# Performance work log

Measured on AMD Instinct MI355X. Metric: run time of the kernel, lower is better.

## Reference

```python
import jax, jax.numpy as jnp
import numpy as np

G, P, PO, TAU = 4, 32, 128, 2.0  # n_groups, spatial_points, out_points=P*out_multiplier, level-softmax temperature
STRIDES = (4.0, 8.0, 16.0, 32.0)
EPS = 1e-5

def _ln2(x):
    # LayerNorm over last two dims, no affine (F.layer_norm(x, x.shape[-2:]))
    mu = jnp.mean(x, axis=(-2, -1), keepdims=True)
    var = jnp.var(x, axis=(-2, -1), keepdims=True)
    return (x - mu) * jax.lax.rsqrt(var + EPS)

def _ln1(x, g, b):
    mu = jnp.mean(x, axis=-1, keepdims=True)
    var = jnp.var(x, axis=-1, keepdims=True)
    return (x - mu) * jax.lax.rsqrt(var + EPS) * g + b

def _bilinear(feat, xp, yp):
    # feat: (B,G,H,W,Ce); xp,yp: (B,N,G,P) pixel coords; grid_sample bilinear,
    # zero padding, align_corners=False semantics.
    B, Gg, H, W, Ce = feat.shape
    x0 = jnp.floor(xp); y0 = jnp.floor(yp)
    wx1 = xp - x0; wy1 = yp - y0
    b_idx = jnp.arange(B)[:, None, None, None]
    g_idx = jnp.arange(Gg)[None, None, :, None]
    def gather(xi, yi):
        valid = (xi >= 0) & (xi < W) & (yi >= 0) & (yi < H)
        xc = jnp.clip(xi, 0, W - 1).astype(jnp.int32)
        yc = jnp.clip(yi, 0, H - 1).astype(jnp.int32)
        return feat[b_idx, g_idx, yc, xc] * valid[..., None]
    v00 = gather(x0, y0); v10 = gather(x0 + 1.0, y0)
    v01 = gather(x0, y0 + 1.0); v11 = gather(x0 + 1.0, y0 + 1.0)
    wx0 = 1.0 - wx1; wy0 = 1.0 - wy1
    return (v00 * (wx0 * wy0)[..., None] + v10 * (wx1 * wy0)[..., None]
            + v01 * (wx0 * wy1)[..., None] + v11 * (wx1 * wy1)[..., None])

def _forward(queries, xyzr, feats, W_off, b_off, W_param, b_param, W_out, b_out, gamma, beta):
    B, N, D = queries.shape
    Ce = feats[0].shape[1] // G  # 64 channels per group
    # learned offsets -> sample points (make_sample_points)
    offset = (queries @ W_off + b_off).reshape(B, N, G, P, 3)
    xy = xyzr[..., :2]
    z = xyzr[..., 2]
    r = xyzr[..., 3:4]
    roi_wh = (2.0 ** xyzr[..., 2:3]) * (2.0 ** jnp.concatenate([-0.5 * r, 0.5 * r], axis=-1))  # (B,N,2)
    sample_xy = xy[:, :, None, None, :] + offset[..., :2] * roi_wh[:, :, None, None, :]  # (B,N,G,P,2)
    sample_z = z[:, :, None, None] + offset[..., 2]  # (B,N,G,P) log2 scale
    # soft level assignment across the FPN pyramid
    lvl_log = jnp.log2(jnp.asarray(STRIDES, dtype=queries.dtype))
    lw = jax.nn.softmax(-((sample_z[..., None] - lvl_log) ** 2) / TAU, axis=-1)  # (B,N,G,P,L)
    # SAMPLE4D (image mode, T=1): multi-scale group-wise bilinear gather, level-weighted sum
    sampled = jnp.zeros((B, N, G, P, Ce), queries.dtype)
    for l, feat in enumerate(feats):
        H, W = feat.shape[-2:]
        featg = feat.reshape(B, G, Ce, H, W).transpose(0, 1, 3, 4, 2)  # (B,G,H,W,Ce)
        xp = sample_xy[..., 0] / STRIDES[l] - 0.5
        yp = sample_xy[..., 1] / STRIDES[l] - 0.5
        sampled = sampled + _bilinear(featg, xp, yp) * lw[..., l, None]
    # AdaptiveMixing: per-query generated channel-mix M and point-mix S
    params = (queries @ W_param + b_param).reshape(B, N, G, -1)
    M = params[..., :Ce * Ce].reshape(B, N, G, Ce, Ce)
    S = params[..., Ce * Ce:].reshape(B, N, G, PO, P)
    h = jnp.einsum('bngpc,bngcd->bngpd', sampled, M)  # channel mixing
    h = jax.nn.relu(_ln2(h))
    h = jnp.einsum('bngqp,bngpd->bngqd', S, h)        # point mixing -> (B,N,G,PO,Ce)
    h = jax.nn.relu(_ln2(h))
    h = h.reshape(B, N, G * PO * Ce)
    q = queries + h @ W_out + b_out  # out_proj + residual
    return _ln1(q, gamma, beta)      # norm_s

def setup_inputs() -> dict:
    key = jax.random.key(0)
    ks = jax.random.split(key, 12)
    B, N, D, C = 2, 300, 256, 256
    HW = [(200, 336), (100, 168), (50, 84), (25, 42)]
    inp = {}
    inp['queries'] = jax.random.normal(ks[0], (B, N, D), jnp.float32)
    u = jax.random.uniform(ks[1], (B, N, 4), jnp.float32)
    inp['xyzr'] = jnp.stack([u[..., 0] * 1344.0, u[..., 1] * 800.0,
                             2.0 + 3.0 * u[..., 2], u[..., 3] - 0.5], axis=-1)
    for i, (H, W) in enumerate(HW):
        inp[f'feat{i}'] = jax.random.normal(ks[2 + i], (B, C, H, W), jnp.float32)
    npar = G * (64 * 64 + PO * P)  # 32768
    inp['W_off'] = jax.random.normal(ks[6], (D, G * P * 3), jnp.float32) * 0.02
    inp['b_off'] = jax.random.normal(ks[7], (G * P * 3,), jnp.float32) * 0.1
    inp['W_param'] = jax.random.normal(ks[8], (D, npar), jnp.float32) * (1.0 / np.sqrt(D))
    inp['b_param'] = jnp.zeros((npar,), jnp.float32)
    inp['W_out'] = jax.random.normal(ks[9], (G * PO * 64, D), jnp.float32) * (1.0 / np.sqrt(G * PO * 64))
    inp['b_out'] = jnp.zeros((D,), jnp.float32)
    inp['gamma'] = jnp.ones((D,), jnp.float32)
    inp['beta'] = jnp.zeros((D,), jnp.float32)
    return inp

def reference(queries, xyzr, feat0, feat1, feat2, feat3, W_off, b_off, W_param, b_param, W_out, b_out, gamma, beta):
    return _forward(queries, xyzr, (feat0, feat1, feat2, feat3),
                    W_off, b_off, W_param, b_param, W_out, b_out, gamma, beta)
```

## Files before the change

kernel.cpp:

```cpp
#include <hip/hip_runtime.h>
#include <hip/hip_bf16.h>

typedef short bf16x8 __attribute__((ext_vector_type(8)));
typedef float f32x4 __attribute__((ext_vector_type(4)));
typedef unsigned short u16x4 __attribute__((ext_vector_type(4)));

#define NQ 600
#define D 256
#define NPAR 32768
#define EPS 1e-5f
#define KSPLIT 32

#define OFF_OFFS     ((size_t)0)
#define OFF_QB       ((size_t)1048576)
#define OFF_WOFFT    ((size_t)1441792)
#define OFF_H        ((size_t)2097152)
#define OFF_WPT      ((size_t)2097152)
#define OFF_PARAMS   ((size_t)41418752)
#define OFF_KPART    ((size_t)41418752)
#define OFF_WOT      ((size_t)80740352)
#define OFF_FEATT    ((size_t)97517568)

#define PIX_PER_BG 89250

__device__ __forceinline__ void gload_lds16(const void* g, void* l) {
    __builtin_amdgcn_global_load_lds((const __attribute__((address_space(1))) unsigned int*)g,
                                     (__attribute__((address_space(3))) unsigned int*)l,
                                     16, 0, 0);
}
__device__ __forceinline__ float bf2f(unsigned short us) {
    union { unsigned u; float f; } cv; cv.u = ((unsigned)us) << 16; return cv.f;
}
__device__ __forceinline__ unsigned short f2bf(float f) {
    __hip_bfloat16 h = __float2bfloat16(f);
    return *(unsigned short*)&h;
}

__global__ __launch_bounds__(256) void k_mega_prep(
        const float* __restrict__ f0, const float* __restrict__ f1,
        const float* __restrict__ f2, const float* __restrict__ f3,
        const float* __restrict__ W_param, const float* __restrict__ W_out,
        const float* __restrict__ W_off, const float* __restrict__ q,
        __hip_bfloat16* __restrict__ featT,
        __hip_bfloat16* __restrict__ Wpt, __hip_bfloat16* __restrict__ Wot,
        __hip_bfloat16* __restrict__ Wofft, __hip_bfloat16* __restrict__ qb) {
    __shared__ __align__(16) float tile[64 * 66];
    int bidf = blockIdx.x;
    int t = threadIdx.x;
    if (bidf < 13000) {
        int bg = bidf / 1625, r = bidf % 1625;
        const float* in; int H, W, lvloff, y, x0;
        if (r < 1200)      { in = f0; H = 200; W = 336; lvloff = 0;     y = r / 6;  x0 = (r % 6) * 64; }
        else if (r < 1500) { r -= 1200; in = f1; H = 100; W = 168; lvloff = 67200; y = r / 3; x0 = (r % 3) * 64; }
        else if (r < 1600) { r -= 1500; in = f2; H = 50;  W = 84;  lvloff = 84000; y = r >> 1; x0 = (r & 1) * 64; }
        else               { r -= 1600; in = f3; H = 25;  W = 42;  lvloff = 88200; y = r;     x0 = 0; }
        int b = bg >> 2, g = bg & 3;
        const float* inb = in + ((size_t)(b * 256 + g * 64) * H + y) * W + x0;
        size_t HW = (size_t)H * W;
        #pragma unroll
        for (int rr = 0; rr < 8; rr++) {
            int qq = t + 256 * rr;
            int c = qq >> 5, xl = (qq & 31) * 2;
            if (x0 + xl < W) {
                float2 v = *(const float2*)(inb + (size_t)c * HW + xl);
                *(float2*)(tile + c * 66 + xl) = v;
            }
        }
        __syncthreads();
        __hip_bfloat16* ob = featT + ((size_t)bg * PIX_PER_BG + lvloff + (size_t)y * W + x0) * 64;
        #pragma unroll
        for (int r2 = 0; r2 < 2; r2++) {
            int task = t + 256 * r2;
            int xl = task >> 3, c8 = (task & 7) * 8;
            if (x0 + xl < W) {
                unsigned short o[8];
                #pragma unroll
                for (int i = 0; i < 8; i++) o[i] = f2bf(tile[(c8 + i) * 66 + xl]);
                *(bf16x8*)(ob + (size_t)xl * 64 + c8) = *(bf16x8*)o;
            }
        }
        return;
    }
    int idx = bidf - 13000;
    if (idx >= 16480) {
        int i = (idx - 16480) * 2048 + t * 8;
        float4 v0 = *(const float4*)(q + i);
        float4 v1 = *(const float4*)(q + i + 4);
        unsigned short o[8];
        o[0] = f2bf(v0.x); o[1] = f2bf(v0.y); o[2] = f2bf(v0.z); o[3] = f2bf(v0.w);
        o[4] = f2bf(v1.x); o[5] = f2bf(v1.y); o[6] = f2bf(v1.z); o[7] = f2bf(v1.w);
        *(bf16x8*)(qb + i) = *(bf16x8*)o;
        return;
    }
    const float* in; __hip_bfloat16* out; int R, C, bx, by;
    if (idx < 8192)       { in = W_param; out = Wpt;   R = 256;   C = 32768; bx = idx & 1023; by = idx >> 10; }
    else if (idx < 16384) { idx -= 8192;  in = W_out;  out = Wot; R = 32768; C = 256; bx = idx & 7; by = idx >> 3; }
    else                  { idx -= 16384; in = W_off;  out = Wofft; R = 256; C = 384; bx = idx % 12; by = idx / 12; }
    float (*tt)[33] = (float(*)[33])tile;
    int tx = t & 31, ty = t >> 5;
    int c = bx * 32 + tx;
    #pragma unroll
    for (int i = 0; i < 4; i++) {
        int rr = by * 32 + ty + i * 8;
        float v = 0.f;
        if (rr < R && c < C) v = in[(size_t)rr * C + c];
        tt[ty + i * 8][tx] = v;
    }
    __syncthreads();
    int r2 = by * 32 + tx;
    #pragma unroll
    for (int i = 0; i < 4; i++) {
        int c2 = bx * 32 + ty + i * 8;
        if (c2 < C && r2 < R) out[(size_t)c2 * R + r2] = __float2bfloat16(tt[tx][ty + i * 8]);
    }
}

__global__ __launch_bounds__(256) void k_gemm1_offs(const __hip_bfloat16* __restrict__ A,
                              const __hip_bfloat16* __restrict__ WofftB, const __hip_bfloat16* __restrict__ WptB,
                              const float* __restrict__ b_off, const float* __restrict__ b_param,
                              float* __restrict__ offs, __hip_bfloat16* __restrict__ params) {
    __shared__ __align__(16) char ldsB[65536];
    int id = blockIdx.x;
    bool isOff = id < 15;
    int m0, n0;
    const __hip_bfloat16* Bt;
    const float* bias;
    if (isOff) { m0 = (id % 5) * 128; n0 = (id / 5) * 128; Bt = WofftB; bias = b_off; }
    else { int i2 = id - 15; m0 = (i2 % 5) * 128; n0 = (i2 / 5) * 128; Bt = WptB; bias = b_param; }
    int t = threadIdx.x;
    int lane = t & 63, w = t >> 6;
    int la = lane & 15, lb = lane >> 4;

    const char* Bg = (const char*)Bt;
    #pragma unroll
    for (int r = 0; r < 16; r++) {
        int p = (r * 4 + w) * 64 + lane;
        int row = p >> 5, c16 = p & 31;
        int c16s = c16 ^ (row & 7);
        gload_lds16(Bg + (size_t)(n0 + row) * 512 + c16s * 16, ldsB + p * 16);
    }
    bf16x8 a[2][8];
    #pragma unroll
    for (int mi = 0; mi < 2; mi++) {
        int row = m0 + w * 32 + mi * 16 + la;
        row = row < NQ ? row : NQ - 1;
        #pragma unroll
        for (int ks = 0; ks < 8; ks++)
            a[mi][ks] = *(const bf16x8*)(A + (size_t)row * 256 + ks * 32 + lb * 8);
    }
    f32x4 acc[2][8];
    #pragma unroll
    for (int i = 0; i < 2; i++)
        #pragma unroll
        for (int j = 0; j < 8; j++) acc[i][j] = (f32x4)(0.f);
    __syncthreads();

    #pragma unroll
    for (int ks = 0; ks < 8; ks++) {
        bf16x8 b[8];
        #pragma unroll
        for (int ni = 0; ni < 8; ni++) {
            int row = ni * 16 + la;
            int c16s = (ks * 4 + lb) ^ (row & 7);
            b[ni] = *(const bf16x8*)(ldsB + row * 512 + c16s * 16);
        }
        #pragma unroll
        for (int mi = 0; mi < 2; mi++)
            #pragma unroll
            for (int ni = 0; ni < 8; ni++)
                acc[mi][ni] = __builtin_amdgcn_mfma_f32_16x16x32_bf16(a[mi][ks], b[ni], acc[mi][ni], 0, 0, 0);
    }
    #pragma unroll
    for (int mi = 0; mi < 2; mi++) {
        int rbase = m0 + w * 32 + mi * 16 + lb * 4;
        #pragma unroll
        for (int ni = 0; ni < 8; ni++) {
            int col = n0 + ni * 16 + la;
            float bv = bias[col];
            #pragma unroll
            for (int rg = 0; rg < 4; rg++) {
                int row = rbase + rg;
                if (row < NQ) {
                    if (isOff) offs[(size_t)row * 384 + col] = acc[mi][ni][rg] + bv;
                    else params[(size_t)row * NPAR + col] = __float2bfloat16(acc[mi][ni][rg] + bv);
                }
            }
        }
    }
}

#define MIX_SMP 0
#define MIX_MT  4096
#define MIX_SS  12288
#define MIX_H1T 20480
__device__ inline float2 blk_reduce2(float s, float ss, float* red, float norm) {
    __syncthreads();
    #pragma unroll
    for (int off = 32; off; off >>= 1) { s += __shfl_down(s, off); ss += __shfl_down(ss, off); }
    int wave = threadIdx.x >> 6, lane = threadIdx.x & 63;
    if (lane == 0) { red[wave * 2] = s; red[wave * 2 + 1] = ss; }
    __syncthreads();
    if (threadIdx.x == 0) {
        float a = 0.f, b = 0.f;
        #pragma unroll
        for (int i = 0; i < 4; i++) { a += red[2 * i]; b += red[2 * i + 1]; }
        red[8] = a * norm; red[9] = b * norm;
    }
    __syncthreads();
    return make_float2(red[8], red[9]);
}

__global__ __launch_bounds__(256) void k_sample_mix(const float* __restrict__ offs,
                      const float* __restrict__ xyzr,
                      const __hip_bfloat16* __restrict__ featT,
                      const __hip_bfloat16* __restrict__ params,
                      __hip_bfloat16* __restrict__ h) {
    __shared__ __align__(16) char lds[24576];
    __shared__ float smeta[32][8];
    __shared__ float red[16];
    int bid = blockIdx.x;
    int m = bid >> 2, g = bid & 3;
    int b = m / 300;
    int t = threadIdx.x;
    int lane = t & 63, w = t >> 6;
    int la = lane & 15, lb = lane >> 4;
    const __hip_bfloat16* pbase = params + (size_t)m * NPAR + g * 8192;

    #pragma unroll
    for (int r = 0; r < 2; r++) {
        int i = t + r * 256;
        int c = i >> 3, d0 = (i & 7) * 8;
        bf16x8 v = *(const bf16x8*)(pbase + i * 8);
        #pragma unroll
        for (int j = 0; j < 8; j++) {
            int d = d0 + j;
            int addr = MIX_MT + d * 128 + ((c >> 3) ^ (d & 7)) * 16 + (c & 7) * 2;
            *(unsigned short*)(lds + addr) = ((unsigned short*)&v)[j];
        }
    }
    #pragma unroll
    for (int r = 0; r < 2; r++) {
        int i = t + r * 256;
        int qr = i >> 2, c16 = i & 3;
        bf16x8 v = *(const bf16x8*)(pbase + 4096 + i * 8);
        *(bf16x8*)(lds + MIX_SS + qr * 64 + (c16 ^ (qr & 3)) * 16) = v;
    }
    if (t < 32) {
        int p = t;
        const float* op = offs + (size_t)m * 384 + (g * 32 + p) * 3;
        float o0 = op[0], o1 = op[1], o2 = op[2];
        float cx = xyzr[m * 4 + 0], cy = xyzr[m * 4 + 1], z = xyzr[m * 4 + 2], rr = xyzr[m * 4 + 3];
        smeta[p][0] = cx + o0 * exp2f(z - 0.5f * rr);
        smeta[p][1] = cy + o1 * exp2f(z + 0.5f * rr);
        float sz = z + o2;
        float e[4], mx = -1e30f;
        #pragma unroll
        for (int l = 0; l < 4; l++) { float d = sz - (float)(2 + l); e[l] = -0.5f * d * d; mx = fmaxf(mx, e[l]); }
        float ssum = 0.f;
        #pragma unroll
        for (int l = 0; l < 4; l++) { e[l] = __expf(e[l] - mx); ssum += e[l]; }
        float inv = 1.f / ssum;
        #pragma unroll
        for (int l = 0; l < 4; l++) smeta[p][2 + l] = e[l] * inv;
    }
    __syncthreads();

    int corner = lane >> 4;
    int dx = corner & 1, dy = corner >> 1;
    int ch = (lane & 15) * 4;
    const int Hs[4] = {200, 100, 50, 25};
    const int Ws[4] = {336, 168, 84, 42};
    const int Ls[4] = {0, 67200, 84000, 88200};
    const float invS[4] = {0.25f, 0.125f, 0.0625f, 0.03125f};
    const __hip_bfloat16* base_bg = featT + (size_t)(b * 4 + g) * PIX_PER_BG * 64;
    for (int pi = 0; pi < 8; pi++) {
        int p = w * 8 + pi;
        float sx = smeta[p][0], sy = smeta[p][1];
        float acc0 = 0.f, acc1 = 0.f, acc2 = 0.f, acc3 = 0.f;
        #pragma unroll
        for (int l = 0; l < 4; l++) {
            float wl = smeta[p][2 + l];
            if (wl < 1e-6f) continue;
            const int H = Hs[l], W = Ws[l];
            float xp = sx * invS[l] - 0.5f, yp = sy * invS[l] - 0.5f;
            float x0f = floorf(xp), y0f = floorf(yp);
            float wx1 = xp - x0f, wy1 = yp - y0f;
            int xi = (int)x0f + dx, yi = (int)y0f + dy;
            bool valid = (xi >= 0) && (xi < W) && (yi >= 0) && (yi < H);
            int xc = xi < 0 ? 0 : (xi >= W ? W - 1 : xi);
            int yc = yi < 0 ? 0 : (yi >= H ? H - 1 : yi);
            float cw = (dx ? wx1 : 1.f - wx1) * (dy ? wy1 : 1.f - wy1) * wl;
            if (!valid) cw = 0.f;
            const __hip_bfloat16* src = base_bg + ((size_t)Ls[l] + (size_t)yc * W + xc) * 64 + ch;
            u16x4 v = *(const u16x4*)src;
            acc0 += cw * bf2f(v[0]);
            acc1 += cw * bf2f(v[1]);
            acc2 += cw * bf2f(v[2]);
            acc3 += cw * bf2f(v[3]);
        }
        acc0 += __shfl_xor(acc0, 16); acc1 += __shfl_xor(acc1, 16);
        acc2 += __shfl_xor(acc2, 16); acc3 += __shfl_xor(acc3, 16);
        acc0 += __shfl_xor(acc0, 32); acc1 += __shfl_xor(acc1, 32);
        acc2 += __shfl_xor(acc2, 32); acc3 += __shfl_xor(acc3, 32);
        if (lane < 16) {
            unsigned short o[4];
            o[0] = f2bf(acc0); o[1] = f2bf(acc1); o[2] = f2bf(acc2); o[3] = f2bf(acc3);
            int slot = lane >> 1, half = lane & 1;
            *(u16x4*)(lds + MIX_SMP + p * 128 + ((slot ^ (p & 7)) * 16) + half * 8) = *(u16x4*)o;
        }
    }
    __syncthreads();

    f32x4 acc1v[2];
    acc1v[0] = (f32x4)(0.f); acc1v[1] = (f32x4)(0.f);
    int dcol = w * 16 + la;
    #pragma unroll
    for (int ks = 0; ks < 2; ks++) {
        bf16x8 bfr = *(const bf16x8*)(lds + MIX_MT + dcol * 128 + (((ks * 4 + lb)) ^ (dcol & 7)) * 16);
        #pragma unroll
        for (int mi = 0; mi < 2; mi++) {
            int prow = mi * 16 + la;
            bf16x8 afr = *(const bf16x8*)(lds + MIX_SMP + prow * 128 + ((ks * 4 + lb) ^ (prow & 7)) * 16);
            acc1v[mi] = __builtin_amdgcn_mfma_f32_16x16x32_bf16(afr, bfr, acc1v[mi], 0, 0, 0);
        }
    }
    float s = 0.f, ss = 0.f;
    #pragma unroll
    for (int mi = 0; mi < 2; mi++)
        #pragma unroll
        for (int j = 0; j < 4; j++) { float v = acc1v[mi][j]; s += v; ss += v * v; }
    float2 r1 = blk_reduce2(s, ss, red, 1.f / 2048.f);
    float mu = r1.x, inv = rsqrtf(r1.y - r1.x * r1.x + EPS);
    #pragma unroll
    for (int mi = 0; mi < 2; mi++) {
        u16x4 pk;
        #pragma unroll
        for (int rg = 0; rg < 4; rg++) {
            float v = (acc1v[mi][rg] - mu) * inv;
            pk[rg] = f2bf(v > 0.f ? v : 0.f);
        }
        int c16 = mi * 2 + (lb >> 1);
        int off8 = 8 * (lb & 1);
        *(u16x4*)(lds + MIX_H1T + dcol * 64 + ((c16 ^ (dcol & 3)) * 16) + off8) = pk;
    }
    __syncthreads();

    f32x4 acc2v[8];
    bf16x8 bfr2 = *(const bf16x8*)(lds + MIX_H1T + dcol * 64 + ((lb ^ (dcol & 3)) * 16));
    #pragma unroll
    for (int nj = 0; nj < 8; nj++) {
        int qrow = nj * 16 + la;
        bf16x8 afr = *(const bf16x8*)(lds + MIX_SS + qrow * 64 + ((lb ^ (qrow & 3)) * 16));
        acc2v[nj] = __builtin_amdgcn_mfma_f32_16x16x32_bf16(afr, bfr2, (f32x4)(0.f), 0, 0, 0);
    }
    s = 0.f; ss = 0.f;
    #pragma unroll
    for (int nj = 0; nj < 8; nj++)
        #pragma unroll
        for (int j = 0; j < 4; j++) { float v = acc2v[nj][j]; s += v; ss += v * v; }
    float2 r2 = blk_reduce2(s, ss, red, 1.f / 8192.f);
    float mu2 = r2.x, inv2 = rsqrtf(r2.y - r2.x * r2.x + EPS);
    __hip_bfloat16* hb = h + (size_t)m * NPAR + g * 8192;
    #pragma unroll
    for (int nj = 0; nj < 8; nj++) {
        #pragma unroll
        for (int rg = 0; rg < 4; rg++) {
            int qr = nj * 16 + lb * 4 + rg;
            float v = (acc2v[nj][rg] - mu2) * inv2;
            v = v > 0.f ? v : 0.f;
            hb[qr * 64 + dcol] = __float2bfloat16(v);
        }
    }
}

__global__ __launch_bounds__(256) void k_gemm_out(const __hip_bfloat16* __restrict__ A,
                           const __hip_bfloat16* __restrict__ Bt, float* __restrict__ kpart) {
    __shared__ __align__(16) char lds[49152];
    int n0 = blockIdx.x * 128, m0 = blockIdx.y * 64;
    size_t k0 = (size_t)blockIdx.z * 1024;
    int t = threadIdx.x, lane = t & 63, w = t >> 6;
    int la = lane & 15, lb = lane >> 4;
    int wm = w >> 1, wn = w & 1;

    const char* Ag = (const char*)A;
    const char* Bg = (const char*)Bt;

    auto stage = [&](int buf, int st) {
        size_t kk = k0 + (size_t)st * 64;
        char* dstA = lds + buf * 24576;
        char* dstB = dstA + 8192;
        #pragma unroll
        for (int r = 0; r < 2; r++) {
            int p = (r * 4 + w) * 64 + lane;
            int row = p >> 3, c16 = p & 7;
            int c16s = c16 ^ (row & 7);
            int grow = m0 + row; grow = grow < NQ ? grow : NQ - 1;
            gload_lds16(Ag + ((size_t)grow * NPAR + kk) * 2 + c16s * 16, dstA + p * 16);
        }
        #pragma unroll
        for (int r = 0; r < 4; r++) {
            int p = (r * 4 + w) * 64 + lane;
            int row = p >> 3, c16 = p & 7;
            int c16s = c16 ^ (row & 7);
            gload_lds16(Bg + ((size_t)(n0 + row) * NPAR + kk) * 2 + c16s * 16, dstB + p * 16);
        }
    };

    f32x4 acc[2][4];
    #pragma unroll
    for (int i = 0; i < 2; i++)
        #pragma unroll
        for (int j = 0; j < 4; j++) acc[i][j] = (f32x4)(0.f);

    stage(0, 0);
    __syncthreads();
    for (int st = 0; st < 16; st++) {
        int buf = st & 1;
        if (st < 15) stage(buf ^ 1, st + 1);
        const char* tA = lds + buf * 24576;
        const char* tB = tA + 8192;
        #pragma unroll
        for (int ks = 0; ks < 2; ks++) {
            bf16x8 a[2], b[4];
            #pragma unroll
            for (int mi = 0; mi < 2; mi++) {
                int row = wm * 32 + mi * 16 + la;
                int c16s = (ks * 4 + lb) ^ (row & 7);
                a[mi] = *(const bf16x8*)(tA + row * 128 + c16s * 16);
            }
            #pragma unroll
            for (int ni = 0; ni < 4; ni++) {
                int row = wn * 64 + ni * 16 + la;
                int c16s = (ks * 4 + lb) ^ (row & 7);
                b[ni] = *(const bf16x8*)(tB + row * 128 + c16s * 16);
            }
            #pragma unroll
            for (int mi = 0; mi < 2; mi++)
                #pragma unroll
                for (int ni = 0; ni < 4; ni++)
                    acc[mi][ni] = __builtin_amdgcn_mfma_f32_16x16x32_bf16(a[mi], b[ni], acc[mi][ni], 0, 0, 0);
        }
        __syncthreads();
    }

    float* outp = kpart + (size_t)blockIdx.z * (NQ * D);
    #pragma unroll
    for (int mi = 0; mi < 2; mi++) {
        int rbase = m0 + wm * 32 + mi * 16 + lb * 4;
        #pragma unroll
        for (int ni = 0; ni < 4; ni++) {
            int col = n0 + wn * 64 + ni * 16 + la;
            #pragma unroll
            for (int rg = 0; rg < 4; rg++) {
                int row = rbase + rg;
                if (row < NQ) outp[(size_t)row * D + col] = acc[mi][ni][rg];
            }
        }
    }
}

__global__ void k_ln_out(const float* __restrict__ kpart, const float* __restrict__ queries,
                         const float* __restrict__ b_out, const float* __restrict__ gamma,
                         const float* __restrict__ beta, float* __restrict__ out) {
    int m = blockIdx.x, t = threadIdx.x;
    float x = queries[m * 256 + t] + b_out[t];
    for (int kc = 0; kc < KSPLIT; kc++) x += kpart[(size_t)kc * (NQ * D) + m * 256 + t];
    __shared__ float red[16];
    float s = x, ss = x * x;
    #pragma unroll
    for (int off = 32; off; off >>= 1) { s += __shfl_down(s, off); ss += __shfl_down(ss, off); }
    int wave = t >> 6, lane = t & 63;
    if (lane == 0) { red[wave * 2] = s; red[wave * 2 + 1] = ss; }
    __syncthreads();
    if (t == 0) {
        float a = 0.f, b = 0.f;
        #pragma unroll
        for (int i = 0; i < 4; i++) { a += red[2 * i]; b += red[2 * i + 1]; }
        red[8] = a * (1.f / 256.f); red[9] = b * (1.f / 256.f);
    }
    __syncthreads();
    float mu = red[8], var = red[9] - mu * mu;
    float inv = rsqrtf(var + EPS);
    out[m * 256 + t] = (x - mu) * inv * gamma[t] + beta[t];
}

extern "C" void kernel_launch(void* const* d_in, const int* in_sizes, int n_in,
                              void* d_out, int out_size, void* d_ws, size_t ws_size,
                              hipStream_t stream) {
    const float* queries = (const float*)d_in[0];
    const float* xyzr    = (const float*)d_in[1];
    const float* f0      = (const float*)d_in[2];
    const float* f1      = (const float*)d_in[3];
    const float* f2      = (const float*)d_in[4];
    const float* f3      = (const float*)d_in[5];
    const float* W_off   = (const float*)d_in[6];
    const float* b_off   = (const float*)d_in[7];
    const float* W_param = (const float*)d_in[8];
    const float* b_param = (const float*)d_in[9];
    const float* W_out   = (const float*)d_in[10];
    const float* b_out   = (const float*)d_in[11];
    const float* gamma   = (const float*)d_in[12];
    const float* beta    = (const float*)d_in[13];
    float* out = (float*)d_out;
    char* ws = (char*)d_ws;

    float* offs            = (float*)(ws + OFF_OFFS);
    __hip_bfloat16* qb     = (__hip_bfloat16*)(ws + OFF_QB);
    __hip_bfloat16* Wofft  = (__hip_bfloat16*)(ws + OFF_WOFFT);
    __hip_bfloat16* hbuf   = (__hip_bfloat16*)(ws + OFF_H);
    __hip_bfloat16* Wpt    = (__hip_bfloat16*)(ws + OFF_WPT);
    __hip_bfloat16* params = (__hip_bfloat16*)(ws + OFF_PARAMS);
    float* kpart           = (float*)(ws + OFF_KPART);
    __hip_bfloat16* Wot    = (__hip_bfloat16*)(ws + OFF_WOT);
    __hip_bfloat16* featT  = (__hip_bfloat16*)(ws + OFF_FEATT);

    k_mega_prep<<<29555, 256, 0, stream>>>(f0, f1, f2, f3, W_param, W_out, W_off, queries,
                                           featT, Wpt, Wot, Wofft, qb);
    k_gemm1_offs<<<1295, 256, 0, stream>>>(qb, Wofft, Wpt, b_off, b_param, offs, params);
    k_sample_mix<<<2400, 256, 0, stream>>>(offs, xyzr, featT, params, hbuf);
    k_gemm_out<<<dim3(2, 10, KSPLIT), 256, 0, stream>>>(hbuf, Wot, kpart);
    k_ln_out<<<600, 256, 0, stream>>>(kpart, queries, b_out, gamma, beta, out);
}
```

Before: 205.0 us.

## Shrink transpose and GEMM1 tiles, remap gemm_out blocks across XCDs

The feature-transpose tiles drop from 64 to 32 pixels wide, and the output stores become 4-byte pairs instead of 16-byte vectors. The first GEMM now uses 128x64 output tiles with half the LDS, which doubles the block count to raise occupancy and parallelism. gemm_out moves to a 1D grid with a block index swizzle meant to spread work across the XCDs. The narrower stores in the transpose may lower write efficiency, and the smaller GEMM tiles reload A more often.

```diff
diff --git a/kernel.cpp b/kernel.cpp
--- a/kernel.cpp
+++ b/kernel.cpp
@@ -44,44 +44,45 @@
         __hip_bfloat16* __restrict__ featT,
         __hip_bfloat16* __restrict__ Wpt, __hip_bfloat16* __restrict__ Wot,
         __hip_bfloat16* __restrict__ Wofft, __hip_bfloat16* __restrict__ qb) {
-    __shared__ __align__(16) float tile[64 * 66];
+    __shared__ __align__(16) float tile[64][33];
     int bidf = blockIdx.x;
     int t = threadIdx.x;
-    if (bidf < 13000) {
-        int bg = bidf / 1625, r = bidf % 1625;
-        const float* in; int H, W, lvloff, y, x0;
-        if (r < 1200)      { in = f0; H = 200; W = 336; lvloff = 0;     y = r / 6;  x0 = (r % 6) * 64; }
-        else if (r < 1500) { r -= 1200; in = f1; H = 100; W = 168; lvloff = 67200; y = r / 3; x0 = (r % 3) * 64; }
-        else if (r < 1600) { r -= 1500; in = f2; H = 50;  W = 84;  lvloff = 84000; y = r >> 1; x0 = (r & 1) * 64; }
-        else               { r -= 1600; in = f3; H = 25;  W = 42;  lvloff = 88200; y = r;     x0 = 0; }
+    if (bidf < 24000) {
+        int bg = bidf / 3000, r = bidf % 3000;
+        const float* in; int H, W, lvloff, y, xt;
+        if (r < 2200)      { in = f0; H = 200; W = 336; lvloff = 0;     xt = r % 11; y = r / 11; }
+        else if (r < 2800) { r -= 2200; in = f1; H = 100; W = 168; lvloff = 67200; xt = r % 6; y = r / 6; }
+        else if (r < 2950) { r -= 2800; in = f2; H = 50;  W = 84;  lvloff = 84000; xt = r % 3; y = r / 3; }
+        else               { r -= 2950; in = f3; H = 25;  W = 42;  lvloff = 88200; xt = r & 1; y = r >> 1; }
+        int x0 = xt * 32;
         int b = bg >> 2, g = bg & 3;
-        const float* inb = in + ((size_t)(b * 256 + g * 64) * H + y) * W + x0;
+        int tx = t & 31, ty = t >> 5;
         size_t HW = (size_t)H * W;
-        #pragma unroll
-        for (int rr = 0; rr < 8; rr++) {
-            int qq = t + 256 * rr;
-            int c = qq >> 5, xl = (qq & 31) * 2;
-            if (x0 + xl < W) {
-                float2 v = *(const float2*)(inb + (size_t)c * HW + xl);
-                *(float2*)(tile + c * 66 + xl) = v;
+        const float* inb = in + ((size_t)(b * 256 + g * 64) * H + y) * W;
+        #pragma unroll
+        for (int i = 0; i < 8; i++) {
+            int c = ty + i * 8;
+            int x = x0 + tx;
+            float v = 0.f;
+            if (x < W) v = inb[(size_t)c * HW + x];
+            tile[c][tx] = v;
+        }
+        __syncthreads();
+        __hip_bfloat16* ob = featT + ((size_t)bg * PIX_PER_BG + lvloff + (size_t)y * W) * 64;
+        #pragma unroll
+        for (int k = 0; k < 4; k++) {
+            int j = t * 2 + k * 512;
+            int x = j >> 6, c = j & 63;
+            if (x0 + x < W) {
+                ushort2 pk;
+                pk.x = f2bf(tile[c][x]);
+                pk.y = f2bf(tile[c + 1][x]);
+                *(ushort2*)(ob + (size_t)(x0 + x) * 64 + c) = pk;
             }
         }
-        __syncthreads();
-        __hip_bfloat16* ob = featT + ((size_t)bg * PIX_PER_BG + lvloff + (size_t)y * W + x0) * 64;
-        #pragma unroll
-        for (int r2 = 0; r2 < 2; r2++) {
-            int task = t + 256 * r2;
-            int xl = task >> 3, c8 = (task & 7) * 8;
-            if (x0 + xl < W) {
-                unsigned short o[8];
-                #pragma unroll
-                for (int i = 0; i < 8; i++) o[i] = f2bf(tile[(c8 + i) * 66 + xl]);
-                *(bf16x8*)(ob + (size_t)xl * 64 + c8) = *(bf16x8*)o;
-            }
-        }
         return;
     }
-    int idx = bidf - 13000;
+    int idx = bidf - 24000;
     if (idx >= 16480) {
         int i = (idx - 16480) * 2048 + t * 8;
         float4 v0 = *(const float4*)(q + i);
@@ -119,21 +120,21 @@
                               const __hip_bfloat16* __restrict__ WofftB, const __hip_bfloat16* __restrict__ WptB,
                               const float* __restrict__ b_off, const float* __restrict__ b_param,
                               float* __restrict__ offs, __hip_bfloat16* __restrict__ params) {
-    __shared__ __align__(16) char ldsB[65536];
+    __shared__ __align__(16) char ldsB[32768];
     int id = blockIdx.x;
-    bool isOff = id < 15;
+    bool isOff = id < 30;
     int m0, n0;
     const __hip_bfloat16* Bt;
     const float* bias;
-    if (isOff) { m0 = (id % 5) * 128; n0 = (id / 5) * 128; Bt = WofftB; bias = b_off; }
-    else { int i2 = id - 15; m0 = (i2 % 5) * 128; n0 = (i2 / 5) * 128; Bt = WptB; bias = b_param; }
+    if (isOff) { m0 = (id % 5) * 128; n0 = (id / 5) * 64; Bt = WofftB; bias = b_off; }
+    else { int i2 = id - 30; m0 = (i2 % 5) * 128; n0 = (i2 / 5) * 64; Bt = WptB; bias = b_param; }
     int t = threadIdx.x;
     int lane = t & 63, w = t >> 6;
     int la = lane & 15, lb = lane >> 4;
 
     const char* Bg = (const char*)Bt;
     #pragma unroll
-    for (int r = 0; r < 16; r++) {
+    for (int r = 0; r < 8; r++) {
         int p = (r * 4 + w) * 64 + lane;
         int row = p >> 5, c16 = p & 31;
         int c16s = c16 ^ (row & 7);
@@ -148,18 +149,18 @@
         for (int ks = 0; ks < 8; ks++)
             a[mi][ks] = *(const bf16x8*)(A + (size_t)row * 256 + ks * 32 + lb * 8);
     }
-    f32x4 acc[2][8];
+    f32x4 acc[2][4];
     #pragma unroll
     for (int i = 0; i < 2; i++)
         #pragma unroll
-        for (int j = 0; j < 8; j++) acc[i][j] = (f32x4)(0.f);
+        for (int j = 0; j < 4; j++) acc[i][j] = (f32x4)(0.f);
     __syncthreads();
 
     #pragma unroll
     for (int ks = 0; ks < 8; ks++) {
-        bf16x8 b[8];
-        #pragma unroll
-        for (int ni = 0; ni < 8; ni++) {
+        bf16x8 b[4];
+        #pragma unroll
+        for (int ni = 0; ni < 4; ni++) {
             int row = ni * 16 + la;
             int c16s = (ks * 4 + lb) ^ (row & 7);
             b[ni] = *(const bf16x8*)(ldsB + row * 512 + c16s * 16);
@@ -167,14 +168,14 @@
         #pragma unroll
         for (int mi = 0; mi < 2; mi++)
             #pragma unroll
-            for (int ni = 0; ni < 8; ni++)
+            for (int ni = 0; ni < 4; ni++)
                 acc[mi][ni] = __builtin_amdgcn_mfma_f32_16x16x32_bf16(a[mi][ks], b[ni], acc[mi][ni], 0, 0, 0);
     }
     #pragma unroll
     for (int mi = 0; mi < 2; mi++) {
         int rbase = m0 + w * 32 + mi * 16 + lb * 4;
         #pragma unroll
-        for (int ni = 0; ni < 8; ni++) {
+        for (int ni = 0; ni < 4; ni++) {
             int col = n0 + ni * 16 + la;
             float bv = bias[col];
             #pragma unroll
@@ -376,8 +377,14 @@
 __global__ __launch_bounds__(256) void k_gemm_out(const __hip_bfloat16* __restrict__ A,
                            const __hip_bfloat16* __restrict__ Bt, float* __restrict__ kpart) {
     __shared__ __align__(16) char lds[49152];
-    int n0 = blockIdx.x * 128, m0 = blockIdx.y * 64;
-    size_t k0 = (size_t)blockIdx.z * 1024;
+    int bid = blockIdx.x;
+    int work = (bid & 7) * 80 + (bid >> 3);
+    int mblk = work % 10;
+    int nz = work / 10;
+    int n0 = (nz & 1) * 128;
+    int z = nz >> 1;
+    int m0 = mblk * 64;
+    size_t k0 = (size_t)z * 1024;
     int t = threadIdx.x, lane = t & 63, w = t >> 6;
     int la = lane & 15, lb = lane >> 4;
     int wm = w >> 1, wn = w & 1;
@@ -443,7 +450,7 @@
         __syncthreads();
     }
 
-    float* outp = kpart + (size_t)blockIdx.z * (NQ * D);
+    float* outp = kpart + (size_t)z * (NQ * D);
     #pragma unroll
     for (int mi = 0; mi < 2; mi++) {
         int rbase = m0 + wm * 32 + mi * 16 + lb * 4;
@@ -514,10 +521,10 @@
     __hip_bfloat16* Wot    = (__hip_bfloat16*)(ws + OFF_WOT);
     __hip_bfloat16* featT  = (__hip_bfloat16*)(ws + OFF_FEATT);
 
-    k_mega_prep<<<29555, 256, 0, stream>>>(f0, f1, f2, f3, W_param, W_out, W_off, queries,
+    k_mega_prep<<<40555, 256, 0, stream>>>(f0, f1, f2, f3, W_param, W_out, W_off, queries,
                                            featT, Wpt, Wot, Wofft, qb);
-    k_gemm1_offs<<<1295, 256, 0, stream>>>(qb, Wofft, Wpt, b_off, b_param, offs, params);
+    k_gemm1_offs<<<2590, 256, 0, stream>>>(qb, Wofft, Wpt, b_off, b_param, offs, params);
     k_sample_mix<<<2400, 256, 0, stream>>>(offs, xyzr, featT, params, hbuf);
-    k_gemm_out<<<dim3(2, 10, KSPLIT), 256, 0, stream>>>(hbuf, Wot, kpart);
+    k_gemm_out<<<640, 256, 0, stream>>>(hbuf, Wot, kpart);
     k_ln_out<<<600, 256, 0, stream>>>(kpart, queries, b_out, gamma, beta, out);
 }
```

Result: slower. 216.8 us (+5.8%).
